# Kernel tuning notes

Measured on AMD Instinct MI355X. Metric: run time of the kernel, lower is better.

The kernel has to match this reference:

```python
import jax, jax.numpy as jnp
import numpy as np

D_MODEL = 1024
D_FF = 4096
N_EXPERTS = 8
D_EXPERT = D_FF // N_EXPERTS  # 512
TOP_K = 2
LB_WEIGHT = 0.01
B, S = 4, 2048


def setup_inputs() -> dict:
    key = jax.random.key(0)
    ks = jax.random.split(key, 8)
    x = jax.random.normal(ks[0], (B, S, D_MODEL), dtype=jnp.float32)
    # per-expert FFN params stacked on expert axis
    w1 = jax.random.normal(ks[1], (N_EXPERTS, D_MODEL, D_EXPERT), dtype=jnp.float32) * (1.0 / np.sqrt(D_MODEL))
    b1 = jnp.zeros((N_EXPERTS, D_EXPERT), dtype=jnp.float32)
    w2 = jax.random.normal(ks[2], (N_EXPERTS, D_EXPERT, D_MODEL), dtype=jnp.float32) * (1.0 / np.sqrt(D_EXPERT))
    b2 = jnp.zeros((N_EXPERTS, D_MODEL), dtype=jnp.float32)
    centroids = jax.random.normal(ks[3], (N_EXPERTS, D_MODEL), dtype=jnp.float32) * 0.02
    w_route = jax.random.normal(ks[4], (N_EXPERTS, D_MODEL), dtype=jnp.float32) * (1.0 / np.sqrt(D_MODEL))
    return {"x": x, "w1": w1, "b1": b1, "w2": w2, "b2": b2,
            "centroids": centroids, "w_route": w_route}


def _top_k_softmax(logits, k):
    # softmax restricted to the top-k logits per token; zeros elsewhere
    vals, _ = jax.lax.top_k(logits, k)          # (..., k)
    thresh = vals[..., -1:]                     # kth-largest value
    masked = jnp.where(logits >= thresh, logits, -jnp.inf)
    return jax.nn.softmax(masked, axis=-1)


def reference(x, w1, b1, w2, b2, centroids, w_route):
    eps = 1e-12
    x_norm = x / jnp.maximum(jnp.linalg.norm(x, axis=-1, keepdims=True), eps)
    c_norm = centroids / jnp.maximum(jnp.linalg.norm(centroids, axis=-1, keepdims=True), eps)
    cos_scores = jnp.einsum('bsd,ed->bse', x_norm, c_norm)
    route_scores = jnp.einsum('bsd,ed->bse', x, w_route)
    logits = cos_scores + route_scores                       # (B,S,E)
    gates = _top_k_softmax(logits, TOP_K)                    # (B,S,E)
    # all experts computed on all tokens (dense MoE, masked combine)
    h = jax.nn.gelu(jnp.einsum('bsd,edh->bseh', x, w1) + b1, approximate=False)
    expert_out = jnp.einsum('bseh,ehd->bsed', h, w2) + b2    # (B,S,E,D)
    out = jnp.einsum('bse,bsed->bsd', gates, expert_out)
    return out
```

## Files before the change

### kernel.cpp

```cpp
#include <hip/hip_runtime.h>
#include <hip/hip_bf16.h>
#include <math.h>

#define T_TOK 8192
#define DM 1024
#define DE 512
#define NE 8
#define DFF 4096

#define CO_X   0
#define CO_W1  8388608
#define CO_W2  12582912
#define CO_B1  16777216
#define CO_B2  16781312
#define CO_CE  16789504
#define CO_WR  16797696
#define CO_TOT 16805888

#define WS_GATE2 256
#define WS_B32   65792
#define WS_TOP2  262400
#define WS_TOK   295168
#define WS_AE    360704
#define WS_AG    426240
#define WS_INV   491776
#define WS_CONV  557312
#define WS_HC    34169088
#define WS_OC    50946304

typedef __attribute__((ext_vector_type(8))) __bf16 bf16x8;
typedef __attribute__((ext_vector_type(4))) __bf16 bf16x4;
typedef __attribute__((ext_vector_type(4))) float f32x4;

__device__ __forceinline__ f32x4 ld4(const void* p, size_t off, int md)
{
  f32x4 r;
  if (md){
    bf16x4 v = *(const bf16x4*)((const __bf16*)p + off);
    #pragma unroll
    for (int j = 0; j < 4; j++) r[j] = (float)v[j];
  } else {
    r = *(const f32x4*)((const float*)p + off);
  }
  return r;
}

__device__ __forceinline__ void async_ld16(const __bf16* g, __bf16* l)
{
  __builtin_amdgcn_global_load_lds(
      (const __attribute__((address_space(1))) unsigned int*)g,
      (__attribute__((address_space(3))) unsigned int*)l, 16, 0, 0);
}

__global__ __launch_bounds__(256) void detect_k(const void* xp, const void* cp,
                                                int* meta, int* b32)
{
  const int tid = threadIdx.x;
  const float* xf = (const float*)xp;
  int ok = 0;
  for (int i = tid; i < 1024; i += 256){
    float a = fabsf(xf[i]);
    if (a > 1e-8f && a < 100.f) ok++;
  }
  __shared__ int cnt;
  __shared__ int flg;
  if (tid == 0) cnt = 0;
  __syncthreads();
  atomicAdd(&cnt, ok);
  __syncthreads();
  if (tid == 0){ flg = (cnt > 512) ? 0 : 1; meta[0] = flg; }
  __syncthreads();
  const int md = flg;

  const int e = tid >> 5, i = tid & 31;
  float ss = 0.f;
  for (int j = 0; j < 32; j++){
    size_t d = (size_t)e * DM + i + j * 32;
    float v = md ? (float)((const __bf16*)cp)[d] : ((const float*)cp)[d];
    ss += v * v;
  }
  #pragma unroll
  for (int m = 1; m < 32; m <<= 1) ss += __shfl_xor(ss, m, 64);
  float* cinv = (float*)(meta + 48);
  if (i == 0) cinv[e] = 1.f / fmaxf(sqrtf(ss), 1e-12f);

  b32[tid] = 0;
  if (tid < 8) meta[16 + tid] = 0;
}

__global__ __launch_bounds__(256) void convert_k(
    const float* __restrict__ b1, const float* __restrict__ b2,
    const float* __restrict__ ce, const float* __restrict__ wr,
    __bf16* __restrict__ dst, const int* __restrict__ meta)
{
  if (meta[0]) return;
  const size_t j = ((size_t)blockIdx.x * 256 + threadIdx.x) * 4;
  const float* src;
  const size_t doff = CO_B1 + j;
  if      (j < 4096)  src = b1 + j;
  else if (j < 12288) src = b2 + (j - 4096);
  else if (j < 20480) src = ce + (j - 12288);
  else                src = wr + (j - 20480);
  f32x4 v = *(const f32x4*)src;
  bf16x4 o;
  #pragma unroll
  for (int t = 0; t < 4; t++) o[t] = (__bf16)v[t];
  *(bf16x4*)(dst + doff) = o;
}

__global__ __launch_bounds__(256) void transp_k(
    const void* w1q, const void* w2q, __bf16* __restrict__ conv,
    const int* __restrict__ meta)
{
  const int md = meta[0];
  __shared__ __bf16 tile[32][33];
  const int b = blockIdx.x, tid = threadIdx.x;
  const int ty = tid >> 5, tx = tid & 31;

  const void* src; __bf16* dst; int ldS, ldD, i0, j0; size_t soff, doffb;
  if (b < 4096){
    const int e = b >> 9, t = b & 511;
    i0 = (t >> 4) << 5; j0 = (t & 15) << 5;
    ldS = DE; ldD = DM;
    soff = (size_t)e * DM * DE;
    dst = conv + CO_W1; doffb = (size_t)e * DE * DM;
    src = md ? (const void*)((const __bf16*)w1q) : (const void*)((const float*)w1q);
  } else {
    const int e = (b - 4096) >> 9, t = (b - 4096) & 511;
    i0 = (t >> 5) << 5; j0 = (t & 31) << 5;
    ldS = DM; ldD = DE;
    soff = (size_t)e * DE * DM;
    dst = conv + CO_W2; doffb = (size_t)e * DM * DE;
    src = md ? (const void*)((const __bf16*)w2q) : (const void*)((const float*)w2q);
  }

  #pragma unroll
  for (int rr = 0; rr < 4; rr++){
    const int r = rr * 8 + ty;
    const size_t s = soff + (size_t)(i0 + r) * ldS + j0 + tx;
    tile[r][tx] = md ? ((const __bf16*)src)[s] : (__bf16)((const float*)src)[s];
  }
  __syncthreads();
  #pragma unroll
  for (int rr = 0; rr < 4; rr++){
    const int r = rr * 8 + ty;
    dst[doffb + (size_t)(j0 + r) * ldD + i0 + tx] = tile[tx][r];
  }
}

__global__ __launch_bounds__(256) void route_k(
    const void* __restrict__ xp, const void* __restrict__ cp,
    const void* __restrict__ wp, const int* __restrict__ meta,
    __bf16* __restrict__ conv, float2* __restrict__ gate2,
    int* __restrict__ top2, int* __restrict__ b32)
{
  const int md = meta[0];
  const float* cinv = (const float*)(meta + 48);
  const int tid = threadIdx.x;
  const int g = tid >> 4, l = tid & 15;
  const int t = blockIdx.x * 16 + g;

  __shared__ int hist[8];
  if (tid < 8) hist[tid] = 0;
  __syncthreads();

  float xx = 0.f, cd[NE], wd[NE];
  #pragma unroll
  for (int e = 0; e < NE; e++){ cd[e] = 0.f; wd[e] = 0.f; }

  const size_t xbase = (size_t)t * DM;
  for (int j = 0; j < 16; j++){
    const int d0 = j * 64 + l * 4;
    f32x4 xv = ld4(xp, xbase + d0, md);
    if (!md){
      bf16x4 o;
      #pragma unroll
      for (int jj = 0; jj < 4; jj++) o[jj] = (__bf16)xv[jj];
      *(bf16x4*)(conv + CO_X + xbase + d0) = o;
    }
    xx += xv[0]*xv[0] + xv[1]*xv[1] + xv[2]*xv[2] + xv[3]*xv[3];
    #pragma unroll
    for (int e = 0; e < NE; e++){
      f32x4 cv = ld4(cp, (size_t)e * DM + d0, md);
      f32x4 wv = ld4(wp, (size_t)e * DM + d0, md);
      cd[e] += xv[0]*cv[0] + xv[1]*cv[1] + xv[2]*cv[2] + xv[3]*cv[3];
      wd[e] += xv[0]*wv[0] + xv[1]*wv[1] + xv[2]*wv[2] + xv[3]*wv[3];
    }
  }
  #pragma unroll
  for (int m = 1; m < 16; m <<= 1){
    xx += __shfl_xor(xx, m, 64);
    #pragma unroll
    for (int e = 0; e < NE; e++){
      cd[e] += __shfl_xor(cd[e], m, 64);
      wd[e] += __shfl_xor(wd[e], m, 64);
    }
  }

  if (l == 0){
    const float rxn = 1.f / fmaxf(sqrtf(xx), 1e-12f);
    float logits[NE];
    #pragma unroll
    for (int e = 0; e < NE; e++) logits[e] = cd[e] * rxn * cinv[e] + wd[e];
    float m1 = -1e30f; int i1 = 0;
    #pragma unroll
    for (int e = 0; e < NE; e++) if (logits[e] > m1){ m1 = logits[e]; i1 = e; }
    float m2 = -1e30f; int i2 = (i1 == 0) ? 1 : 0;
    #pragma unroll
    for (int e = 0; e < NE; e++)
      if (e != i1 && logits[e] > m2){ m2 = logits[e]; i2 = e; }
    float denom = 0.f, ex1 = 0.f, ex2 = 0.f;
    #pragma unroll
    for (int e = 0; e < NE; e++){
      if (logits[e] >= m2){
        float ee = expf(logits[e] - m1);
        denom += ee;
        if (e == i1) ex1 = ee;
        if (e == i2) ex2 = ee;
      }
    }
    const float inv = 1.f / denom;
    gate2[t] = make_float2(ex1 * inv, ex2 * inv);
    top2[t] = i1 | (i2 << 8);
    atomicAdd(&hist[i1], 1);
    atomicAdd(&hist[i2], 1);
  }
  __syncthreads();
  if (tid < 8) atomicAdd(&b32[(blockIdx.x >> 4) * 8 + tid], hist[tid]);
}

__global__ void offsets_k(int* meta, int* b32)
{
  const int l = threadIdx.x;
  int running = 0;
  for (int e = 0; e < NE; e++){
    int v = (l < 32) ? b32[l * 8 + e] : 0;
    int incl = v;
    #pragma unroll
    for (int ofs = 1; ofs < 32; ofs <<= 1){
      int n = __shfl_up(incl, ofs, 64);
      if (l >= ofs) incl += n;
    }
    int tot = __shfl(incl, 31, 64);
    if (l < 32) b32[l * 8 + e] = running + (incl - v);
    if (l == 0){ meta[16 + e] = tot; meta[32 + e] = running; }
    running += tot;
  }
}

__global__ __launch_bounds__(256) void place_k(
    const int* __restrict__ top2, const float2* __restrict__ gate2,
    const int* __restrict__ b32, int* __restrict__ tok, int* __restrict__ ae,
    float* __restrict__ agv, int* __restrict__ inv)
{
  __shared__ int cur[8];
  if (threadIdx.x < 8) cur[threadIdx.x] = b32[blockIdx.x * 8 + threadIdx.x];
  __syncthreads();
  const int t = blockIdx.x * 256 + threadIdx.x;
  const int p = top2[t];
  const float2 gg = gate2[t];
  const int e1 = p & 255, e2 = (p >> 8) & 255;
  const int s1 = atomicAdd(&cur[e1], 1);
  tok[s1] = t; ae[s1] = e1; agv[s1] = gg.x; inv[2 * t] = s1;
  const int s2 = atomicAdd(&cur[e2], 1);
  tok[s2] = t; ae[s2] = e2; agv[s2] = gg.y; inv[2 * t + 1] = s2;
}

__device__ __forceinline__ bool find_tile(const int* meta, int tm,
                                          int& e, int& base, int& valid)
{
  for (e = 0; e < NE; e++){
    const int cnt = meta[16 + e];
    const int nt = (cnt + 127) >> 7;
    if (tm < nt){
      const int r0 = tm << 7;
      base = meta[32 + e] + r0;
      valid = cnt - r0;
      return true;
    }
    tm -= nt;
  }
  return false;
}

__global__ __launch_bounds__(512, 4) void gemm1g_k(
    const void* xq, const void* b1q, const __bf16* __restrict__ conv,
    const int* __restrict__ meta, const int* __restrict__ tok,
    const float* __restrict__ agv, __bf16* __restrict__ Hc)
{
  const int md = meta[0];
  const __bf16* X  = md ? (const __bf16*)xq : conv + CO_X;
  const __bf16* WT = conv + CO_W1;
  const __bf16* bb = md ? (const __bf16*)b1q : conv + CO_B1;

  int e, base, valid;
  if (!find_tile(meta, blockIdx.x, e, base, valid)) return;
  const int n0 = blockIdx.y * 128;

  __shared__ __attribute__((aligned(16))) __bf16 As[2][128 * 32];
  __shared__ __attribute__((aligned(16))) __bf16 Bs[2][128 * 32];

  const int tid = threadIdx.x;
  const int wv = tid >> 6, lane = tid & 63;
  const int q = lane >> 4, ln = lane & 15;
  const int wm = (wv >> 2) * 64, wn = (wv & 3) * 32;
  f32x4 acc[4][2] = {};

  const int sr = tid >> 2, sc = (tid & 3) * 8;
  const int tr = tok[base + ((sr < valid) ? sr : 0)];
  const __bf16* Ag = X + (size_t)tr * DM + sc;
  const __bf16* Bg = WT + (size_t)e * (DE * DM) + (size_t)(n0 + sr) * DM + sc;

  async_ld16(Ag, &As[0][tid * 8]);
  async_ld16(Bg, &Bs[0][tid * 8]);
  __syncthreads();

  int cr = 0;
  for (int k0 = 0; k0 < DM; k0 += 32){
    const int k1 = k0 + 32;
    if (k1 < DM){
      async_ld16(Ag + k1, &As[cr ^ 1][tid * 8]);
      async_ld16(Bg + k1, &Bs[cr ^ 1][tid * 8]);
    }
    bf16x8 af[4], bfr[2];
    #pragma unroll
    for (int mi = 0; mi < 4; mi++)
      af[mi] = *(const bf16x8*)&As[cr][(wm + mi * 16 + ln) * 32 + q * 8];
    #pragma unroll
    for (int ni = 0; ni < 2; ni++)
      bfr[ni] = *(const bf16x8*)&Bs[cr][(wn + ni * 16 + ln) * 32 + q * 8];
    #pragma unroll
    for (int mi = 0; mi < 4; mi++)
      #pragma unroll
      for (int ni = 0; ni < 2; ni++)
        acc[mi][ni] = __builtin_amdgcn_mfma_f32_16x16x32_bf16(
            af[mi], bfr[ni], acc[mi][ni], 0, 0, 0);
    __syncthreads();
    cr ^= 1;
  }

  const int coln = n0 + wn;
  float bset[2];
  #pragma unroll
  for (int ni = 0; ni < 2; ni++)
    bset[ni] = (float)bb[e * DE + coln + ni * 16 + ln];
  #pragma unroll
  for (int mi = 0; mi < 4; mi++){
    #pragma unroll
    for (int r = 0; r < 4; r++){
      const int row = wm + mi * 16 + q * 4 + r;
      if (row < valid){
        const int slot = base + row;
        const float g = agv[slot];
        #pragma unroll
        for (int ni = 0; ni < 2; ni++){
          float v = acc[mi][ni][r] + bset[ni];
          float h = 0.5f * v * (1.0f + erff(v * 0.70710678118654752f));
          Hc[(size_t)slot * DE + coln + ni * 16 + ln] = (__bf16)(g * h);
        }
      }
    }
  }
}

__global__ __launch_bounds__(512, 4) void gemm2g_k(
    const __bf16* __restrict__ Hc, const __bf16* __restrict__ conv,
    const int* __restrict__ meta, __bf16* __restrict__ Oc)
{
  const __bf16* WT = conv + CO_W2;

  int e, base, valid;
  if (!find_tile(meta, blockIdx.x, e, base, valid)) return;
  const int n0 = blockIdx.y * 128;

  __shared__ __attribute__((aligned(16))) __bf16 As[2][128 * 32];
  __shared__ __attribute__((aligned(16))) __bf16 Bs[2][128 * 32];

  const int tid = threadIdx.x;
  const int wv = tid >> 6, lane = tid & 63;
  const int q = lane >> 4, ln = lane & 15;
  const int wm = (wv >> 2) * 64, wn = (wv & 3) * 32;
  f32x4 acc[4][2] = {};

  const int sr = tid >> 2, sc = (tid & 3) * 8;
  const int rc = (sr < valid) ? sr : 0;
  const __bf16* Ag = Hc + (size_t)(base + rc) * DE + sc;
  const __bf16* Bg = WT + (size_t)e * (DM * DE) + (size_t)(n0 + sr) * DE + sc;

  async_ld16(Ag, &As[0][tid * 8]);
  async_ld16(Bg, &Bs[0][tid * 8]);
  __syncthreads();

  int cr = 0;
  for (int k0 = 0; k0 < DE; k0 += 32){
    const int k1 = k0 + 32;
    if (k1 < DE){
      async_ld16(Ag + k1, &As[cr ^ 1][tid * 8]);
      async_ld16(Bg + k1, &Bs[cr ^ 1][tid * 8]);
    }
    bf16x8 af[4], bfr[2];
    #pragma unroll
    for (int mi = 0; mi < 4; mi++)
      af[mi] = *(const bf16x8*)&As[cr][(wm + mi * 16 + ln) * 32 + q * 8];
    #pragma unroll
    for (int ni = 0; ni < 2; ni++)
      bfr[ni] = *(const bf16x8*)&Bs[cr][(wn + ni * 16 + ln) * 32 + q * 8];
    #pragma unroll
    for (int mi = 0; mi < 4; mi++)
      #pragma unroll
      for (int ni = 0; ni < 2; ni++)
        acc[mi][ni] = __builtin_amdgcn_mfma_f32_16x16x32_bf16(
            af[mi], bfr[ni], acc[mi][ni], 0, 0, 0);
    __syncthreads();
    cr ^= 1;
  }

  #pragma unroll
  for (int mi = 0; mi < 4; mi++){
    #pragma unroll
    for (int r = 0; r < 4; r++){
      const int row = wm + mi * 16 + q * 4 + r;
      if (row < valid){
        const int slot = base + row;
        #pragma unroll
        for (int ni = 0; ni < 2; ni++)
          Oc[(size_t)slot * DM + n0 + wn + ni * 16 + ln] = (__bf16)acc[mi][ni][r];
      }
    }
  }
}

__global__ __launch_bounds__(256) void combine_k(
    const __bf16* __restrict__ Oc, const int* __restrict__ inv,
    const int* __restrict__ ae, const float* __restrict__ agv,
    const void* b2q, const int* __restrict__ meta, void* out)
{
  const int md = meta[0];
  const int t = blockIdx.x;
  const int s1 = inv[2 * t], s2 = inv[2 * t + 1];
  const int e1 = ae[s1], e2 = ae[s2];
  const float g1 = agv[s1], g2 = agv[s2];
  const int c = threadIdx.x * 4;

  bf16x4 o1 = *(const bf16x4*)(Oc + (size_t)s1 * DM + c);
  bf16x4 o2 = *(const bf16x4*)(Oc + (size_t)s2 * DM + c);
  f32x4 bv1 = ld4(b2q, (size_t)e1 * DM + c, md);
  f32x4 bv2 = ld4(b2q, (size_t)e2 * DM + c, md);
  f32x4 rr;
  #pragma unroll
  for (int j = 0; j < 4; j++)
    rr[j] = (float)o1[j] + (float)o2[j] + g1 * bv1[j] + g2 * bv2[j];

  if (md){
    bf16x4 ob;
    #pragma unroll
    for (int j = 0; j < 4; j++) ob[j] = (__bf16)rr[j];
    *(bf16x4*)((__bf16*)out + (size_t)t * DM + c) = ob;
  } else {
    *(f32x4*)((float*)out + (size_t)t * DM + c) = rr;
  }
}

extern "C" void kernel_launch(void* const* d_in, const int* in_sizes, int n_in,
                              void* d_out, int out_size, void* d_ws, size_t ws_size,
                              hipStream_t stream)
{
  char* ws = (char*)d_ws;
  int*    meta  = (int*)ws;
  float2* gate2 = (float2*)(ws + WS_GATE2);
  int*    b32   = (int*)(ws + WS_B32);
  int*    top2  = (int*)(ws + WS_TOP2);
  int*    tok   = (int*)(ws + WS_TOK);
  int*    ae    = (int*)(ws + WS_AE);
  float*  agv   = (float*)(ws + WS_AG);
  int*    inv   = (int*)(ws + WS_INV);
  __bf16* conv  = (__bf16*)(ws + WS_CONV);
  __bf16* Hc    = (__bf16*)(ws + WS_HC);
  __bf16* Oc    = (__bf16*)(ws + WS_OC);

  detect_k<<<1, 256, 0, stream>>>(d_in[0], d_in[5], meta, b32);
  transp_k<<<8192, 256, 0, stream>>>(d_in[1], d_in[3], conv, meta);
  convert_k<<<28, 256, 0, stream>>>(
      (const float*)d_in[2], (const float*)d_in[4], (const float*)d_in[5],
      (const float*)d_in[6], conv, meta);
  route_k<<<T_TOK / 16, 256, 0, stream>>>(d_in[0], d_in[5], d_in[6], meta,
                                          conv, gate2, top2, b32);
  offsets_k<<<1, 64, 0, stream>>>(meta, b32);
  place_k<<<T_TOK / 256, 256, 0, stream>>>(top2, gate2, b32, tok, ae, agv, inv);
  gemm1g_k<<<dim3(136, 4), 512, 0, stream>>>(d_in[0], d_in[2], conv, meta,
                                             tok, agv, Hc);
  gemm2g_k<<<dim3(136, 8), 512, 0, stream>>>(Hc, conv, meta, Oc);
  combine_k<<<T_TOK, 256, 0, stream>>>(Oc, inv, ae, agv, d_in[4], meta, d_out);
}
```

Before: 245.4 us.

## Enlarge grouped GEMM tiles to 256x256 and route four tokens per lane group

Both grouped expert GEMMs move from 128x128 to 256x256 output tiles, with each wave computing 128x64 through an 8x4 MFMA accumulator array. Grid sizes shrink to match, and occupancy drops to two blocks per CU. The routing kernel now has each 16-lane group handle four tokens, so the centroid and router weight loads are reused across them. The larger tiles raise arithmetic intensity, but with only about 144 and 288 blocks on 256 CUs, part of the GPU sits idle, register pressure rises, and per-expert padding waste grows.

```diff
diff --git a/kernel.cpp b/kernel.cpp
--- a/kernel.cpp
+++ b/kernel.cpp
@@ -158,50 +158,73 @@
   const float* cinv = (const float*)(meta + 48);
   const int tid = threadIdx.x;
   const int g = tid >> 4, l = tid & 15;
-  const int t = blockIdx.x * 16 + g;
+  const int tbase = blockIdx.x * 64 + g * 4;
 
   __shared__ int hist[8];
   if (tid < 8) hist[tid] = 0;
   __syncthreads();
 
-  float xx = 0.f, cd[NE], wd[NE];
-  #pragma unroll
-  for (int e = 0; e < NE; e++){ cd[e] = 0.f; wd[e] = 0.f; }
-
-  const size_t xbase = (size_t)t * DM;
+  float xx[4] = {0.f, 0.f, 0.f, 0.f};
+  float cd[NE][4], wd[NE][4];
+  #pragma unroll
+  for (int e = 0; e < NE; e++)
+    #pragma unroll
+    for (int tk = 0; tk < 4; tk++){ cd[e][tk] = 0.f; wd[e][tk] = 0.f; }
+
   for (int j = 0; j < 16; j++){
     const int d0 = j * 64 + l * 4;
-    f32x4 xv = ld4(xp, xbase + d0, md);
-    if (!md){
-      bf16x4 o;
-      #pragma unroll
-      for (int jj = 0; jj < 4; jj++) o[jj] = (__bf16)xv[jj];
-      *(bf16x4*)(conv + CO_X + xbase + d0) = o;
-    }
-    xx += xv[0]*xv[0] + xv[1]*xv[1] + xv[2]*xv[2] + xv[3]*xv[3];
+    f32x4 xv[4];
+    #pragma unroll
+    for (int tk = 0; tk < 4; tk++){
+      xv[tk] = ld4(xp, (size_t)(tbase + tk) * DM + d0, md);
+      if (!md){
+        bf16x4 o;
+        #pragma unroll
+        for (int jj = 0; jj < 4; jj++) o[jj] = (__bf16)xv[tk][jj];
+        *(bf16x4*)(conv + CO_X + (size_t)(tbase + tk) * DM + d0) = o;
+      }
+      xx[tk] += xv[tk][0]*xv[tk][0] + xv[tk][1]*xv[tk][1]
+              + xv[tk][2]*xv[tk][2] + xv[tk][3]*xv[tk][3];
+    }
     #pragma unroll
     for (int e = 0; e < NE; e++){
       f32x4 cv = ld4(cp, (size_t)e * DM + d0, md);
       f32x4 wv = ld4(wp, (size_t)e * DM + d0, md);
-      cd[e] += xv[0]*cv[0] + xv[1]*cv[1] + xv[2]*cv[2] + xv[3]*cv[3];
-      wd[e] += xv[0]*wv[0] + xv[1]*wv[1] + xv[2]*wv[2] + xv[3]*wv[3];
+      #pragma unroll
+      for (int tk = 0; tk < 4; tk++){
+        cd[e][tk] += xv[tk][0]*cv[0] + xv[tk][1]*cv[1]
+                   + xv[tk][2]*cv[2] + xv[tk][3]*cv[3];
+        wd[e][tk] += xv[tk][0]*wv[0] + xv[tk][1]*wv[1]
+                   + xv[tk][2]*wv[2] + xv[tk][3]*wv[3];
+      }
     }
   }
   #pragma unroll
   for (int m = 1; m < 16; m <<= 1){
-    xx += __shfl_xor(xx, m, 64);
+    #pragma unroll
+    for (int tk = 0; tk < 4; tk++){
+      xx[tk] += __shfl_xor(xx[tk], m, 64);
+      #pragma unroll
+      for (int e = 0; e < NE; e++){
+        cd[e][tk] += __shfl_xor(cd[e][tk], m, 64);
+        wd[e][tk] += __shfl_xor(wd[e][tk], m, 64);
+      }
+    }
+  }
+
+  if (l < 4){
+    const int t = tbase + l;
+    float xxs = (l == 0) ? xx[0] : (l == 1) ? xx[1] : (l == 2) ? xx[2] : xx[3];
+    float logits[NE];
     #pragma unroll
     for (int e = 0; e < NE; e++){
-      cd[e] += __shfl_xor(cd[e], m, 64);
-      wd[e] += __shfl_xor(wd[e], m, 64);
-    }
-  }
-
-  if (l == 0){
-    const float rxn = 1.f / fmaxf(sqrtf(xx), 1e-12f);
-    float logits[NE];
-    #pragma unroll
-    for (int e = 0; e < NE; e++) logits[e] = cd[e] * rxn * cinv[e] + wd[e];
+      float cds = (l == 0) ? cd[e][0] : (l == 1) ? cd[e][1]
+                : (l == 2) ? cd[e][2] : cd[e][3];
+      float wds = (l == 0) ? wd[e][0] : (l == 1) ? wd[e][1]
+                : (l == 2) ? wd[e][2] : wd[e][3];
+      const float rxn = 1.f / fmaxf(sqrtf(xxs), 1e-12f);
+      logits[e] = cds * rxn * cinv[e] + wds;
+    }
     float m1 = -1e30f; int i1 = 0;
     #pragma unroll
     for (int e = 0; e < NE; e++) if (logits[e] > m1){ m1 = logits[e]; i1 = e; }
@@ -226,7 +249,7 @@
     atomicAdd(&hist[i2], 1);
   }
   __syncthreads();
-  if (tid < 8) atomicAdd(&b32[(blockIdx.x >> 4) * 8 + tid], hist[tid]);
+  if (tid < 8) atomicAdd(&b32[(blockIdx.x >> 2) * 8 + tid], hist[tid]);
 }
 
 __global__ void offsets_k(int* meta, int* b32)
@@ -266,14 +289,14 @@
   tok[s2] = t; ae[s2] = e2; agv[s2] = gg.y; inv[2 * t + 1] = s2;
 }
 
-__device__ __forceinline__ bool find_tile(const int* meta, int tm,
-                                          int& e, int& base, int& valid)
+__device__ __forceinline__ bool find_tile256(const int* meta, int tm,
+                                             int& e, int& base, int& valid)
 {
   for (e = 0; e < NE; e++){
     const int cnt = meta[16 + e];
-    const int nt = (cnt + 127) >> 7;
+    const int nt = (cnt + 255) >> 8;
     if (tm < nt){
-      const int r0 = tm << 7;
+      const int r0 = tm << 8;
       base = meta[32 + e] + r0;
       valid = cnt - r0;
       return true;
@@ -283,7 +306,7 @@
   return false;
 }
 
-__global__ __launch_bounds__(512, 4) void gemm1g_k(
+__global__ __launch_bounds__(512, 2) void gemm1g_k(
     const void* xq, const void* b1q, const __bf16* __restrict__ conv,
     const int* __restrict__ meta, const int* __restrict__ tok,
     const float* __restrict__ agv, __bf16* __restrict__ Hc)
@@ -294,45 +317,52 @@
   const __bf16* bb = md ? (const __bf16*)b1q : conv + CO_B1;
 
   int e, base, valid;
-  if (!find_tile(meta, blockIdx.x, e, base, valid)) return;
-  const int n0 = blockIdx.y * 128;
-
-  __shared__ __attribute__((aligned(16))) __bf16 As[2][128 * 32];
-  __shared__ __attribute__((aligned(16))) __bf16 Bs[2][128 * 32];
+  if (!find_tile256(meta, blockIdx.x, e, base, valid)) return;
+  const int n0 = blockIdx.y * 256;
+
+  __shared__ __attribute__((aligned(16))) __bf16 As[2][256 * 32];
+  __shared__ __attribute__((aligned(16))) __bf16 Bs[2][256 * 32];
 
   const int tid = threadIdx.x;
   const int wv = tid >> 6, lane = tid & 63;
   const int q = lane >> 4, ln = lane & 15;
-  const int wm = (wv >> 2) * 64, wn = (wv & 3) * 32;
-  f32x4 acc[4][2] = {};
+  const int wm = (wv >> 2) * 128, wn = (wv & 3) * 64;
+  f32x4 acc[8][4] = {};
 
   const int sr = tid >> 2, sc = (tid & 3) * 8;
-  const int tr = tok[base + ((sr < valid) ? sr : 0)];
-  const __bf16* Ag = X + (size_t)tr * DM + sc;
-  const __bf16* Bg = WT + (size_t)e * (DE * DM) + (size_t)(n0 + sr) * DM + sc;
-
-  async_ld16(Ag, &As[0][tid * 8]);
-  async_ld16(Bg, &Bs[0][tid * 8]);
+  const int t0 = tok[base + ((sr       < valid) ? sr       : 0)];
+  const int t1 = tok[base + ((sr + 128 < valid) ? sr + 128 : 0)];
+  const __bf16* Ag0 = X + (size_t)t0 * DM + sc;
+  const __bf16* Ag1 = X + (size_t)t1 * DM + sc;
+  const __bf16* Bg0 = WT + (size_t)e * (DE * DM) + (size_t)(n0 + sr) * DM + sc;
+  const __bf16* Bg1 = Bg0 + (size_t)128 * DM;
+
+  async_ld16(Ag0, &As[0][tid * 8]);
+  async_ld16(Ag1, &As[0][tid * 8 + 4096]);
+  async_ld16(Bg0, &Bs[0][tid * 8]);
+  async_ld16(Bg1, &Bs[0][tid * 8 + 4096]);
   __syncthreads();
 
   int cr = 0;
   for (int k0 = 0; k0 < DM; k0 += 32){
     const int k1 = k0 + 32;
     if (k1 < DM){
-      async_ld16(Ag + k1, &As[cr ^ 1][tid * 8]);
-      async_ld16(Bg + k1, &Bs[cr ^ 1][tid * 8]);
-    }
-    bf16x8 af[4], bfr[2];
-    #pragma unroll
-    for (int mi = 0; mi < 4; mi++)
+      async_ld16(Ag0 + k1, &As[cr ^ 1][tid * 8]);
+      async_ld16(Ag1 + k1, &As[cr ^ 1][tid * 8 + 4096]);
+      async_ld16(Bg0 + k1, &Bs[cr ^ 1][tid * 8]);
+      async_ld16(Bg1 + k1, &Bs[cr ^ 1][tid * 8 + 4096]);
+    }
+    bf16x8 af[8], bfr[4];
+    #pragma unroll
+    for (int mi = 0; mi < 8; mi++)
       af[mi] = *(const bf16x8*)&As[cr][(wm + mi * 16 + ln) * 32 + q * 8];
     #pragma unroll
-    for (int ni = 0; ni < 2; ni++)
+    for (int ni = 0; ni < 4; ni++)
       bfr[ni] = *(const bf16x8*)&Bs[cr][(wn + ni * 16 + ln) * 32 + q * 8];
     #pragma unroll
-    for (int mi = 0; mi < 4; mi++)
+    for (int mi = 0; mi < 8; mi++)
       #pragma unroll
-      for (int ni = 0; ni < 2; ni++)
+      for (int ni = 0; ni < 4; ni++)
         acc[mi][ni] = __builtin_amdgcn_mfma_f32_16x16x32_bf16(
             af[mi], bfr[ni], acc[mi][ni], 0, 0, 0);
     __syncthreads();
@@ -340,12 +370,12 @@
   }
 
   const int coln = n0 + wn;
-  float bset[2];
-  #pragma unroll
-  for (int ni = 0; ni < 2; ni++)
+  float bset[4];
+  #pragma unroll
+  for (int ni = 0; ni < 4; ni++)
     bset[ni] = (float)bb[e * DE + coln + ni * 16 + ln];
   #pragma unroll
-  for (int mi = 0; mi < 4; mi++){
+  for (int mi = 0; mi < 8; mi++){
     #pragma unroll
     for (int r = 0; r < 4; r++){
       const int row = wm + mi * 16 + q * 4 + r;
@@ -353,7 +383,7 @@
         const int slot = base + row;
         const float g = agv[slot];
         #pragma unroll
-        for (int ni = 0; ni < 2; ni++){
+        for (int ni = 0; ni < 4; ni++){
           float v = acc[mi][ni][r] + bset[ni];
           float h = 0.5f * v * (1.0f + erff(v * 0.70710678118654752f));
           Hc[(size_t)slot * DE + coln + ni * 16 + ln] = (__bf16)(g * h);
@@ -363,52 +393,59 @@
   }
 }
 
-__global__ __launch_bounds__(512, 4) void gemm2g_k(
+__global__ __launch_bounds__(512, 2) void gemm2g_k(
     const __bf16* __restrict__ Hc, const __bf16* __restrict__ conv,
     const int* __restrict__ meta, __bf16* __restrict__ Oc)
 {
   const __bf16* WT = conv + CO_W2;
 
   int e, base, valid;
-  if (!find_tile(meta, blockIdx.x, e, base, valid)) return;
-  const int n0 = blockIdx.y * 128;
-
-  __shared__ __attribute__((aligned(16))) __bf16 As[2][128 * 32];
-  __shared__ __attribute__((aligned(16))) __bf16 Bs[2][128 * 32];
+  if (!find_tile256(meta, blockIdx.x, e, base, valid)) return;
+  const int n0 = blockIdx.y * 256;
+
+  __shared__ __attribute__((aligned(16))) __bf16 As[2][256 * 32];
+  __shared__ __attribute__((aligned(16))) __bf16 Bs[2][256 * 32];
 
   const int tid = threadIdx.x;
   const int wv = tid >> 6, lane = tid & 63;
   const int q = lane >> 4, ln = lane & 15;
-  const int wm = (wv >> 2) * 64, wn = (wv & 3) * 32;
-  f32x4 acc[4][2] = {};
+  const int wm = (wv >> 2) * 128, wn = (wv & 3) * 64;
+  f32x4 acc[8][4] = {};
 
   const int sr = tid >> 2, sc = (tid & 3) * 8;
-  const int rc = (sr < valid) ? sr : 0;
-  const __bf16* Ag = Hc + (size_t)(base + rc) * DE + sc;
-  const __bf16* Bg = WT + (size_t)e * (DM * DE) + (size_t)(n0 + sr) * DE + sc;
-
-  async_ld16(Ag, &As[0][tid * 8]);
-  async_ld16(Bg, &Bs[0][tid * 8]);
+  const int r0 = (sr       < valid) ? sr       : 0;
+  const int r1 = (sr + 128 < valid) ? sr + 128 : 0;
+  const __bf16* Ag0 = Hc + (size_t)(base + r0) * DE + sc;
+  const __bf16* Ag1 = Hc + (size_t)(base + r1) * DE + sc;
+  const __bf16* Bg0 = WT + (size_t)e * (DM * DE) + (size_t)(n0 + sr) * DE + sc;
+  const __bf16* Bg1 = Bg0 + (size_t)128 * DE;
+
+  async_ld16(Ag0, &As[0][tid * 8]);
+  async_ld16(Ag1, &As[0][tid * 8 + 4096]);
+  async_ld16(Bg0, &Bs[0][tid * 8]);
+  async_ld16(Bg1, &Bs[0][tid * 8 + 4096]);
   __syncthreads();
 
   int cr = 0;
   for (int k0 = 0; k0 < DE; k0 += 32){
     const int k1 = k0 + 32;
     if (k1 < DE){
-      async_ld16(Ag + k1, &As[cr ^ 1][tid * 8]);
-      async_ld16(Bg + k1, &Bs[cr ^ 1][tid * 8]);
-    }
-    bf16x8 af[4], bfr[2];
-    #pragma unroll
-    for (int mi = 0; mi < 4; mi++)
+      async_ld16(Ag0 + k1, &As[cr ^ 1][tid * 8]);
+      async_ld16(Ag1 + k1, &As[cr ^ 1][tid * 8 + 4096]);
+      async_ld16(Bg0 + k1, &Bs[cr ^ 1][tid * 8]);
+      async_ld16(Bg1 + k1, &Bs[cr ^ 1][tid * 8 + 4096]);
+    }
+    bf16x8 af[8], bfr[4];
+    #pragma unroll
+    for (int mi = 0; mi < 8; mi++)
       af[mi] = *(const bf16x8*)&As[cr][(wm + mi * 16 + ln) * 32 + q * 8];
     #pragma unroll
-    for (int ni = 0; ni < 2; ni++)
+    for (int ni = 0; ni < 4; ni++)
       bfr[ni] = *(const bf16x8*)&Bs[cr][(wn + ni * 16 + ln) * 32 + q * 8];
     #pragma unroll
-    for (int mi = 0; mi < 4; mi++)
+    for (int mi = 0; mi < 8; mi++)
       #pragma unroll
-      for (int ni = 0; ni < 2; ni++)
+      for (int ni = 0; ni < 4; ni++)
         acc[mi][ni] = __builtin_amdgcn_mfma_f32_16x16x32_bf16(
             af[mi], bfr[ni], acc[mi][ni], 0, 0, 0);
     __syncthreads();
@@ -416,14 +453,14 @@
   }
 
   #pragma unroll
-  for (int mi = 0; mi < 4; mi++){
+  for (int mi = 0; mi < 8; mi++){
     #pragma unroll
     for (int r = 0; r < 4; r++){
       const int row = wm + mi * 16 + q * 4 + r;
       if (row < valid){
         const int slot = base + row;
         #pragma unroll
-        for (int ni = 0; ni < 2; ni++)
+        for (int ni = 0; ni < 4; ni++)
           Oc[(size_t)slot * DM + n0 + wn + ni * 16 + ln] = (__bf16)acc[mi][ni][r];
       }
     }
@@ -483,12 +520,12 @@
   convert_k<<<28, 256, 0, stream>>>(
       (const float*)d_in[2], (const float*)d_in[4], (const float*)d_in[5],
       (const float*)d_in[6], conv, meta);
-  route_k<<<T_TOK / 16, 256, 0, stream>>>(d_in[0], d_in[5], d_in[6], meta,
+  route_k<<<T_TOK / 64, 256, 0, stream>>>(d_in[0], d_in[5], d_in[6], meta,
                                           conv, gate2, top2, b32);
   offsets_k<<<1, 64, 0, stream>>>(meta, b32);
   place_k<<<T_TOK / 256, 256, 0, stream>>>(top2, gate2, b32, tok, ae, agv, inv);
-  gemm1g_k<<<dim3(136, 4), 512, 0, stream>>>(d_in[0], d_in[2], conv, meta,
-                                             tok, agv, Hc);
-  gemm2g_k<<<dim3(136, 8), 512, 0, stream>>>(Hc, conv, meta, Oc);
+  gemm1g_k<<<dim3(72, 2), 512, 0, stream>>>(d_in[0], d_in[2], conv, meta,
+                                            tok, agv, Hc);
+  gemm2g_k<<<dim3(72, 4), 512, 0, stream>>>(Hc, conv, meta, Oc);
   combine_k<<<T_TOK, 256, 0, stream>>>(Oc, inv, ae, agv, d_in[4], meta, d_out);
 }
```

Result: slower. 332.8 us (+35.6%).

## Deepen GEMM K-tiles to 64 with XOR-swizzled LDS; enlarge gemm2 tiles to 256x256

Applied to the files above, without the earlier changes.

Both grouped expert GEMMs now stage 64-wide K chunks per pipeline step with an XOR swizzle on the LDS layout, halving the number of barriers and aiming to avoid bank conflicts on fragment reads. gemm2 moves to 256x256 output tiles with 8x4 MFMA accumulators per wave and a smaller grid (72x4), raising data reuse per loaded byte. Larger LDS footprints and more accumulator registers lower occupancy (launch bounds drop to 2 blocks). The bigger tiles also waste more rows on partially filled expert tiles and leave fewer blocks to fill the device.

```diff
diff --git a/kernel.cpp b/kernel.cpp
--- a/kernel.cpp
+++ b/kernel.cpp
@@ -283,7 +283,24 @@
   return false;
 }
 
-__global__ __launch_bounds__(512, 4) void gemm1g_k(
+__device__ __forceinline__ bool find_tile256(const int* meta, int tm,
+                                             int& e, int& base, int& valid)
+{
+  for (e = 0; e < NE; e++){
+    const int cnt = meta[16 + e];
+    const int nt = (cnt + 255) >> 8;
+    if (tm < nt){
+      const int r0 = tm << 8;
+      base = meta[32 + e] + r0;
+      valid = cnt - r0;
+      return true;
+    }
+    tm -= nt;
+  }
+  return false;
+}
+
+__global__ __launch_bounds__(512, 2) void gemm1g_k(
     const void* xq, const void* b1q, const __bf16* __restrict__ conv,
     const int* __restrict__ meta, const int* __restrict__ tok,
     const float* __restrict__ agv, __bf16* __restrict__ Hc)
@@ -297,47 +314,65 @@
   if (!find_tile(meta, blockIdx.x, e, base, valid)) return;
   const int n0 = blockIdx.y * 128;
 
-  __shared__ __attribute__((aligned(16))) __bf16 As[2][128 * 32];
-  __shared__ __attribute__((aligned(16))) __bf16 Bs[2][128 * 32];
+  __shared__ __attribute__((aligned(16))) __bf16 As[2][128 * 64];
+  __shared__ __attribute__((aligned(16))) __bf16 Bs[2][128 * 64];
 
   const int tid = threadIdx.x;
   const int wv = tid >> 6, lane = tid & 63;
   const int q = lane >> 4, ln = lane & 15;
   const int wm = (wv >> 2) * 64, wn = (wv & 3) * 32;
+  const int swz = ln & 7;
   f32x4 acc[4][2] = {};
 
-  const int sr = tid >> 2, sc = (tid & 3) * 8;
-  const int tr = tok[base + ((sr < valid) ? sr : 0)];
-  const __bf16* Ag = X + (size_t)tr * DM + sc;
-  const __bf16* Bg = WT + (size_t)e * (DE * DM) + (size_t)(n0 + sr) * DM + sc;
-
-  async_ld16(Ag, &As[0][tid * 8]);
-  async_ld16(Bg, &Bs[0][tid * 8]);
-  __syncthreads();
-
+  const int srow = tid >> 3, sch = tid & 7;
+  const int sx = ((sch ^ (srow & 7)) << 3);
+  const int ta = tok[base + ((srow      < valid) ? srow      : 0)];
+  const int tb = tok[base + ((srow + 64 < valid) ? srow + 64 : 0)];
+  const __bf16* Ag0 = X + (size_t)ta * DM + sx;
+  const __bf16* Ag1 = X + (size_t)tb * DM + sx;
+  const __bf16* Bg0 = WT + (size_t)e * (DE * DM) + (size_t)(n0 + srow) * DM + sx;
+  const __bf16* Bg1 = Bg0 + (size_t)64 * DM;
+
+  #define G1_STAGE(BUF, K0)                                   \
+    do {                                                      \
+      async_ld16(Ag0 + (K0), &As[BUF][tid * 8]);              \
+      async_ld16(Ag1 + (K0), &As[BUF][tid * 8 + 4096]);       \
+      async_ld16(Bg0 + (K0), &Bs[BUF][tid * 8]);              \
+      async_ld16(Bg1 + (K0), &Bs[BUF][tid * 8 + 4096]);       \
+    } while (0)
+
+  #define G1_COMPUTE(BUF)                                                      \
+    do {                                                                       \
+      _Pragma("unroll")                                                        \
+      for (int kk = 0; kk < 2; kk++){                                          \
+        bf16x8 af[4], bfr[2];                                                  \
+        const int ch = (((kk << 2) | q) ^ swz) << 3;                           \
+        _Pragma("unroll")                                                      \
+        for (int mi = 0; mi < 4; mi++)                                         \
+          af[mi] = *(const bf16x8*)&As[BUF][(wm + mi * 16 + ln) * 64 + ch];    \
+        _Pragma("unroll")                                                      \
+        for (int ni = 0; ni < 2; ni++)                                         \
+          bfr[ni] = *(const bf16x8*)&Bs[BUF][(wn + ni * 16 + ln) * 64 + ch];   \
+        _Pragma("unroll")                                                      \
+        for (int mi = 0; mi < 4; mi++)                                         \
+          _Pragma("unroll")                                                    \
+          for (int ni = 0; ni < 2; ni++)                                       \
+            acc[mi][ni] = __builtin_amdgcn_mfma_f32_16x16x32_bf16(             \
+                af[mi], bfr[ni], acc[mi][ni], 0, 0, 0);                        \
+      }                                                                        \
+    } while (0)
+
+  G1_STAGE(0, 0);
+  __syncthreads();
   int cr = 0;
-  for (int k0 = 0; k0 < DM; k0 += 32){
-    const int k1 = k0 + 32;
-    if (k1 < DM){
-      async_ld16(Ag + k1, &As[cr ^ 1][tid * 8]);
-      async_ld16(Bg + k1, &Bs[cr ^ 1][tid * 8]);
-    }
-    bf16x8 af[4], bfr[2];
-    #pragma unroll
-    for (int mi = 0; mi < 4; mi++)
-      af[mi] = *(const bf16x8*)&As[cr][(wm + mi * 16 + ln) * 32 + q * 8];
-    #pragma unroll
-    for (int ni = 0; ni < 2; ni++)
-      bfr[ni] = *(const bf16x8*)&Bs[cr][(wn + ni * 16 + ln) * 32 + q * 8];
-    #pragma unroll
-    for (int mi = 0; mi < 4; mi++)
-      #pragma unroll
-      for (int ni = 0; ni < 2; ni++)
-        acc[mi][ni] = __builtin_amdgcn_mfma_f32_16x16x32_bf16(
-            af[mi], bfr[ni], acc[mi][ni], 0, 0, 0);
+  for (int t = 0; t < 16; ++t){
+    if (t < 15) G1_STAGE(cr ^ 1, (t + 1) * 64);
+    G1_COMPUTE(cr);
     __syncthreads();
     cr ^= 1;
   }
+  #undef G1_STAGE
+  #undef G1_COMPUTE
 
   const int coln = n0 + wn;
   float bset[2];
@@ -363,67 +398,92 @@
   }
 }
 
-__global__ __launch_bounds__(512, 4) void gemm2g_k(
+__global__ __launch_bounds__(512, 2) void gemm2g_k(
     const __bf16* __restrict__ Hc, const __bf16* __restrict__ conv,
     const int* __restrict__ meta, __bf16* __restrict__ Oc)
 {
   const __bf16* WT = conv + CO_W2;
 
   int e, base, valid;
-  if (!find_tile(meta, blockIdx.x, e, base, valid)) return;
-  const int n0 = blockIdx.y * 128;
-
-  __shared__ __attribute__((aligned(16))) __bf16 As[2][128 * 32];
-  __shared__ __attribute__((aligned(16))) __bf16 Bs[2][128 * 32];
+  if (!find_tile256(meta, blockIdx.x, e, base, valid)) return;
+  const int n0 = blockIdx.y * 256;
+
+  __shared__ __attribute__((aligned(16))) __bf16 As[2][256 * 64];
+  __shared__ __attribute__((aligned(16))) __bf16 Bs[2][256 * 64];
 
   const int tid = threadIdx.x;
   const int wv = tid >> 6, lane = tid & 63;
   const int q = lane >> 4, ln = lane & 15;
-  const int wm = (wv >> 2) * 64, wn = (wv & 3) * 32;
-  f32x4 acc[4][2] = {};
-
-  const int sr = tid >> 2, sc = (tid & 3) * 8;
-  const int rc = (sr < valid) ? sr : 0;
-  const __bf16* Ag = Hc + (size_t)(base + rc) * DE + sc;
-  const __bf16* Bg = WT + (size_t)e * (DM * DE) + (size_t)(n0 + sr) * DE + sc;
-
-  async_ld16(Ag, &As[0][tid * 8]);
-  async_ld16(Bg, &Bs[0][tid * 8]);
-  __syncthreads();
-
+  const int wm = (wv >> 2) * 128, wn = (wv & 3) * 64;
+  const int swz = ln & 7;
+  f32x4 acc[8][4] = {};
+
+  const int srow = tid >> 3, sch = tid & 7;
+  const int sx = ((sch ^ (srow & 7)) << 3);
+  const int r0 = (srow       < valid) ? srow       : 0;
+  const int r1 = (srow +  64 < valid) ? srow +  64 : 0;
+  const int r2 = (srow + 128 < valid) ? srow + 128 : 0;
+  const int r3 = (srow + 192 < valid) ? srow + 192 : 0;
+  const __bf16* Ag0 = Hc + (size_t)(base + r0) * DE + sx;
+  const __bf16* Ag1 = Hc + (size_t)(base + r1) * DE + sx;
+  const __bf16* Ag2 = Hc + (size_t)(base + r2) * DE + sx;
+  const __bf16* Ag3 = Hc + (size_t)(base + r3) * DE + sx;
+  const __bf16* Bg0 = WT + (size_t)e * (DM * DE) + (size_t)(n0 + srow) * DE + sx;
+
+  #define G2_STAGE(BUF, K0)                                          \
+    do {                                                             \
+      async_ld16(Ag0 + (K0), &As[BUF][tid * 8]);                     \
+      async_ld16(Ag1 + (K0), &As[BUF][tid * 8 + 4096]);              \
+      async_ld16(Ag2 + (K0), &As[BUF][tid * 8 + 8192]);              \
+      async_ld16(Ag3 + (K0), &As[BUF][tid * 8 + 12288]);             \
+      async_ld16(Bg0 + (K0),                &Bs[BUF][tid * 8]);      \
+      async_ld16(Bg0 + (K0) +  64 * DE,     &Bs[BUF][tid * 8 + 4096]);  \
+      async_ld16(Bg0 + (K0) + 128 * DE,     &Bs[BUF][tid * 8 + 8192]);  \
+      async_ld16(Bg0 + (K0) + 192 * DE,     &Bs[BUF][tid * 8 + 12288]); \
+    } while (0)
+
+  #define G2_COMPUTE(BUF)                                                      \
+    do {                                                                       \
+      _Pragma("unroll")                                                        \
+      for (int kk = 0; kk < 2; kk++){                                          \
+        bf16x8 af[8], bfr[4];                                                  \
+        const int ch = (((kk << 2) | q) ^ swz) << 3;                           \
+        _Pragma("unroll")                                                      \
+        for (int mi = 0; mi < 8; mi++)                                         \
+          af[mi] = *(const bf16x8*)&As[BUF][(wm + mi * 16 + ln) * 64 + ch];    \
+        _Pragma("unroll")                                                      \
+        for (int ni = 0; ni < 4; ni++)                                         \
+          bfr[ni] = *(const bf16x8*)&Bs[BUF][(wn + ni * 16 + ln) * 64 + ch];   \
+        _Pragma("unroll")                                                      \
+        for (int mi = 0; mi < 8; mi++)                                         \
+          _Pragma("unroll")                                                    \
+          for (int ni = 0; ni < 4; ni++)                                       \
+            acc[mi][ni] = __builtin_amdgcn_mfma_f32_16x16x32_bf16(             \
+                af[mi], bfr[ni], acc[mi][ni], 0, 0, 0);                        \
+      }                                                                        \
+    } while (0)
+
+  G2_STAGE(0, 0);
+  __syncthreads();
   int cr = 0;
-  for (int k0 = 0; k0 < DE; k0 += 32){
-    const int k1 = k0 + 32;
-    if (k1 < DE){
-      async_ld16(Ag + k1, &As[cr ^ 1][tid * 8]);
-      async_ld16(Bg + k1, &Bs[cr ^ 1][tid * 8]);
-    }
-    bf16x8 af[4], bfr[2];
-    #pragma unroll
-    for (int mi = 0; mi < 4; mi++)
-      af[mi] = *(const bf16x8*)&As[cr][(wm + mi * 16 + ln) * 32 + q * 8];
-    #pragma unroll
-    for (int ni = 0; ni < 2; ni++)
-      bfr[ni] = *(const bf16x8*)&Bs[cr][(wn + ni * 16 + ln) * 32 + q * 8];
-    #pragma unroll
-    for (int mi = 0; mi < 4; mi++)
-      #pragma unroll
-      for (int ni = 0; ni < 2; ni++)
-        acc[mi][ni] = __builtin_amdgcn_mfma_f32_16x16x32_bf16(
-            af[mi], bfr[ni], acc[mi][ni], 0, 0, 0);
+  for (int t = 0; t < 8; ++t){
+    if (t < 7) G2_STAGE(cr ^ 1, (t + 1) * 64);
+    G2_COMPUTE(cr);
     __syncthreads();
     cr ^= 1;
   }
-
-  #pragma unroll
-  for (int mi = 0; mi < 4; mi++){
+  #undef G2_STAGE
+  #undef G2_COMPUTE
+
+  #pragma unroll
+  for (int mi = 0; mi < 8; mi++){
     #pragma unroll
     for (int r = 0; r < 4; r++){
       const int row = wm + mi * 16 + q * 4 + r;
       if (row < valid){
         const int slot = base + row;
         #pragma unroll
-        for (int ni = 0; ni < 2; ni++)
+        for (int ni = 0; ni < 4; ni++)
           Oc[(size_t)slot * DM + n0 + wn + ni * 16 + ln] = (__bf16)acc[mi][ni][r];
       }
     }
@@ -489,6 +549,6 @@
   place_k<<<T_TOK / 256, 256, 0, stream>>>(top2, gate2, b32, tok, ae, agv, inv);
   gemm1g_k<<<dim3(136, 4), 512, 0, stream>>>(d_in[0], d_in[2], conv, meta,
                                              tok, agv, Hc);
-  gemm2g_k<<<dim3(136, 8), 512, 0, stream>>>(Hc, conv, meta, Oc);
+  gemm2g_k<<<dim3(72, 4), 512, 0, stream>>>(Hc, conv, meta, Oc);
   combine_k<<<T_TOK, 256, 0, stream>>>(Oc, inv, ae, agv, d_in[4], meta, d_out);
 }
```

Measured after the change: 250.5 us. 1.02x slower.

## Widen grouped GEMM tiles to 128x256 and index tiles by expert-interleaved slots

Applied to the files above, without the earlier changes.

Both grouped expert GEMMs move from a 128x128 to a 128x256 output tile, with each wave computing a 64x64 sub-tile (4x4 MFMA accumulators). This doubles the reuse of A-fragment loads per B load and halves the number of column blocks. The tile lookup loop is replaced by a direct mapping, expert = bx&7 and row block = bx>>3, over a fixed 512-wide grid, so many blocks exit early. Occupancy hint drops from 4 to 2 blocks per CU, and register and LDS use rise.

```diff
diff --git a/kernel.cpp b/kernel.cpp
--- a/kernel.cpp
+++ b/kernel.cpp
@@ -266,24 +266,19 @@
   tok[s2] = t; ae[s2] = e2; agv[s2] = gg.y; inv[2 * t + 1] = s2;
 }
 
-__device__ __forceinline__ bool find_tile(const int* meta, int tm,
+__device__ __forceinline__ bool find_slot(const int* meta, int bx,
                                           int& e, int& base, int& valid)
 {
-  for (e = 0; e < NE; e++){
-    const int cnt = meta[16 + e];
-    const int nt = (cnt + 127) >> 7;
-    if (tm < nt){
-      const int r0 = tm << 7;
-      base = meta[32 + e] + r0;
-      valid = cnt - r0;
-      return true;
-    }
-    tm -= nt;
-  }
-  return false;
-}
-
-__global__ __launch_bounds__(512, 4) void gemm1g_k(
+  e = bx & 7;
+  const int cnt = meta[16 + e];
+  const int r0 = (bx >> 3) << 7;
+  if (r0 >= cnt) return false;
+  base = meta[32 + e] + r0;
+  valid = cnt - r0;
+  return true;
+}
+
+__global__ __launch_bounds__(512, 2) void gemm1g_k(
     const void* xq, const void* b1q, const __bf16* __restrict__ conv,
     const int* __restrict__ meta, const int* __restrict__ tok,
     const float* __restrict__ agv, __bf16* __restrict__ Hc)
@@ -294,55 +289,64 @@
   const __bf16* bb = md ? (const __bf16*)b1q : conv + CO_B1;
 
   int e, base, valid;
-  if (!find_tile(meta, blockIdx.x, e, base, valid)) return;
-  const int n0 = blockIdx.y * 128;
+  if (!find_slot(meta, blockIdx.x, e, base, valid)) return;
+  const int n0 = blockIdx.y * 256;
 
   __shared__ __attribute__((aligned(16))) __bf16 As[2][128 * 32];
-  __shared__ __attribute__((aligned(16))) __bf16 Bs[2][128 * 32];
+  __shared__ __attribute__((aligned(16))) __bf16 Bs[2][256 * 32];
 
   const int tid = threadIdx.x;
   const int wv = tid >> 6, lane = tid & 63;
   const int q = lane >> 4, ln = lane & 15;
-  const int wm = (wv >> 2) * 64, wn = (wv & 3) * 32;
-  f32x4 acc[4][2] = {};
+  const int wm = (wv >> 2) * 64, wn = (wv & 3) * 64;
+  f32x4 acc[4][4] = {};
 
   const int sr = tid >> 2, sc = (tid & 3) * 8;
-  const int tr = tok[base + ((sr < valid) ? sr : 0)];
-  const __bf16* Ag = X + (size_t)tr * DM + sc;
-  const __bf16* Bg = WT + (size_t)e * (DE * DM) + (size_t)(n0 + sr) * DM + sc;
-
-  async_ld16(Ag, &As[0][tid * 8]);
-  async_ld16(Bg, &Bs[0][tid * 8]);
-  __syncthreads();
-
+  const int ta = tok[base + ((sr < valid) ? sr : 0)];
+  const __bf16* Ag  = X + (size_t)ta * DM + sc;
+  const __bf16* Bg0 = WT + (size_t)e * (DE * DM) + (size_t)(n0 + sr) * DM + sc;
+  const __bf16* Bg1 = Bg0 + (size_t)128 * DM;
+
+  #define G1_STAGE(BUF, K0)                              \
+    do {                                                 \
+      async_ld16(Ag  + (K0), &As[BUF][tid * 8]);         \
+      async_ld16(Bg0 + (K0), &Bs[BUF][tid * 8]);         \
+      async_ld16(Bg1 + (K0), &Bs[BUF][tid * 8 + 4096]);  \
+    } while (0)
+
+  #define G1_COMPUTE(BUF)                                                      \
+    do {                                                                       \
+      bf16x8 af[4], bfr[4];                                                    \
+      _Pragma("unroll")                                                        \
+      for (int mi = 0; mi < 4; mi++)                                           \
+        af[mi] = *(const bf16x8*)&As[BUF][(wm + mi * 16 + ln) * 32 + q * 8];   \
+      _Pragma("unroll")                                                        \
+      for (int ni = 0; ni < 4; ni++)                                           \
+        bfr[ni] = *(const bf16x8*)&Bs[BUF][(wn + ni * 16 + ln) * 32 + q * 8];  \
+      _Pragma("unroll")                                                        \
+      for (int mi = 0; mi < 4; mi++)                                           \
+        _Pragma("unroll")                                                      \
+        for (int ni = 0; ni < 4; ni++)                                         \
+          acc[mi][ni] = __builtin_amdgcn_mfma_f32_16x16x32_bf16(               \
+              af[mi], bfr[ni], acc[mi][ni], 0, 0, 0);                          \
+    } while (0)
+
+  G1_STAGE(0, 0);
+  __syncthreads();
   int cr = 0;
-  for (int k0 = 0; k0 < DM; k0 += 32){
-    const int k1 = k0 + 32;
-    if (k1 < DM){
-      async_ld16(Ag + k1, &As[cr ^ 1][tid * 8]);
-      async_ld16(Bg + k1, &Bs[cr ^ 1][tid * 8]);
-    }
-    bf16x8 af[4], bfr[2];
-    #pragma unroll
-    for (int mi = 0; mi < 4; mi++)
-      af[mi] = *(const bf16x8*)&As[cr][(wm + mi * 16 + ln) * 32 + q * 8];
-    #pragma unroll
-    for (int ni = 0; ni < 2; ni++)
-      bfr[ni] = *(const bf16x8*)&Bs[cr][(wn + ni * 16 + ln) * 32 + q * 8];
-    #pragma unroll
-    for (int mi = 0; mi < 4; mi++)
-      #pragma unroll
-      for (int ni = 0; ni < 2; ni++)
-        acc[mi][ni] = __builtin_amdgcn_mfma_f32_16x16x32_bf16(
-            af[mi], bfr[ni], acc[mi][ni], 0, 0, 0);
+  for (int t = 0; t < 32; ++t){
+    if (t < 31) G1_STAGE(cr ^ 1, (t + 1) * 32);
+    G1_COMPUTE(cr);
     __syncthreads();
     cr ^= 1;
   }
+  #undef G1_STAGE
+  #undef G1_COMPUTE
 
   const int coln = n0 + wn;
-  float bset[2];
-  #pragma unroll
-  for (int ni = 0; ni < 2; ni++)
+  float bset[4];
+  #pragma unroll
+  for (int ni = 0; ni < 4; ni++)
     bset[ni] = (float)bb[e * DE + coln + ni * 16 + ln];
   #pragma unroll
   for (int mi = 0; mi < 4; mi++){
@@ -353,7 +357,7 @@
         const int slot = base + row;
         const float g = agv[slot];
         #pragma unroll
-        for (int ni = 0; ni < 2; ni++){
+        for (int ni = 0; ni < 4; ni++){
           float v = acc[mi][ni][r] + bset[ni];
           float h = 0.5f * v * (1.0f + erff(v * 0.70710678118654752f));
           Hc[(size_t)slot * DE + coln + ni * 16 + ln] = (__bf16)(g * h);
@@ -363,57 +367,66 @@
   }
 }
 
-__global__ __launch_bounds__(512, 4) void gemm2g_k(
+__global__ __launch_bounds__(512, 2) void gemm2g_k(
     const __bf16* __restrict__ Hc, const __bf16* __restrict__ conv,
     const int* __restrict__ meta, __bf16* __restrict__ Oc)
 {
   const __bf16* WT = conv + CO_W2;
 
   int e, base, valid;
-  if (!find_tile(meta, blockIdx.x, e, base, valid)) return;
-  const int n0 = blockIdx.y * 128;
+  if (!find_slot(meta, blockIdx.x, e, base, valid)) return;
+  const int n0 = blockIdx.y * 256;
 
   __shared__ __attribute__((aligned(16))) __bf16 As[2][128 * 32];
-  __shared__ __attribute__((aligned(16))) __bf16 Bs[2][128 * 32];
+  __shared__ __attribute__((aligned(16))) __bf16 Bs[2][256 * 32];
 
   const int tid = threadIdx.x;
   const int wv = tid >> 6, lane = tid & 63;
   const int q = lane >> 4, ln = lane & 15;
-  const int wm = (wv >> 2) * 64, wn = (wv & 3) * 32;
-  f32x4 acc[4][2] = {};
+  const int wm = (wv >> 2) * 64, wn = (wv & 3) * 64;
+  f32x4 acc[4][4] = {};
 
   const int sr = tid >> 2, sc = (tid & 3) * 8;
-  const int rc = (sr < valid) ? sr : 0;
-  const __bf16* Ag = Hc + (size_t)(base + rc) * DE + sc;
-  const __bf16* Bg = WT + (size_t)e * (DM * DE) + (size_t)(n0 + sr) * DE + sc;
-
-  async_ld16(Ag, &As[0][tid * 8]);
-  async_ld16(Bg, &Bs[0][tid * 8]);
-  __syncthreads();
-
+  const int ra = (sr < valid) ? sr : 0;
+  const __bf16* Ag  = Hc + (size_t)(base + ra) * DE + sc;
+  const __bf16* Bg0 = WT + (size_t)e * (DM * DE) + (size_t)(n0 + sr) * DE + sc;
+  const __bf16* Bg1 = Bg0 + (size_t)128 * DE;
+
+  #define G2_STAGE(BUF, K0)                              \
+    do {                                                 \
+      async_ld16(Ag  + (K0), &As[BUF][tid * 8]);         \
+      async_ld16(Bg0 + (K0), &Bs[BUF][tid * 8]);         \
+      async_ld16(Bg1 + (K0), &Bs[BUF][tid * 8 + 4096]);  \
+    } while (0)
+
+  #define G2_COMPUTE(BUF)                                                      \
+    do {                                                                       \
+      bf16x8 af[4], bfr[4];                                                    \
+      _Pragma("unroll")                                                        \
+      for (int mi = 0; mi < 4; mi++)                                           \
+        af[mi] = *(const bf16x8*)&As[BUF][(wm + mi * 16 + ln) * 32 + q * 8];   \
+      _Pragma("unroll")                                                        \
+      for (int ni = 0; ni < 4; ni++)                                           \
+        bfr[ni] = *(const bf16x8*)&Bs[BUF][(wn + ni * 16 + ln) * 32 + q * 8];  \
+      _Pragma("unroll")                                                        \
+      for (int mi = 0; mi < 4; mi++)                                           \
+        _Pragma("unroll")                                                      \
+        for (int ni = 0; ni < 4; ni++)                                         \
+          acc[mi][ni] = __builtin_amdgcn_mfma_f32_16x16x32_bf16(               \
+              af[mi], bfr[ni], acc[mi][ni], 0, 0, 0);                          \
+    } while (0)
+
+  G2_STAGE(0, 0);
+  __syncthreads();
   int cr = 0;
-  for (int k0 = 0; k0 < DE; k0 += 32){
-    const int k1 = k0 + 32;
-    if (k1 < DE){
-      async_ld16(Ag + k1, &As[cr ^ 1][tid * 8]);
-      async_ld16(Bg + k1, &Bs[cr ^ 1][tid * 8]);
-    }
-    bf16x8 af[4], bfr[2];
-    #pragma unroll
-    for (int mi = 0; mi < 4; mi++)
-      af[mi] = *(const bf16x8*)&As[cr][(wm + mi * 16 + ln) * 32 + q * 8];
-    #pragma unroll
-    for (int ni = 0; ni < 2; ni++)
-      bfr[ni] = *(const bf16x8*)&Bs[cr][(wn + ni * 16 + ln) * 32 + q * 8];
-    #pragma unroll
-    for (int mi = 0; mi < 4; mi++)
-      #pragma unroll
-      for (int ni = 0; ni < 2; ni++)
-        acc[mi][ni] = __builtin_amdgcn_mfma_f32_16x16x32_bf16(
-            af[mi], bfr[ni], acc[mi][ni], 0, 0, 0);
+  for (int t = 0; t < 16; ++t){
+    if (t < 15) G2_STAGE(cr ^ 1, (t + 1) * 32);
+    G2_COMPUTE(cr);
     __syncthreads();
     cr ^= 1;
   }
+  #undef G2_STAGE
+  #undef G2_COMPUTE
 
   #pragma unroll
   for (int mi = 0; mi < 4; mi++){
@@ -423,7 +436,7 @@
       if (row < valid){
         const int slot = base + row;
         #pragma unroll
-        for (int ni = 0; ni < 2; ni++)
+        for (int ni = 0; ni < 4; ni++)
           Oc[(size_t)slot * DM + n0 + wn + ni * 16 + ln] = (__bf16)acc[mi][ni][r];
       }
     }
@@ -487,8 +500,8 @@
                                           conv, gate2, top2, b32);
   offsets_k<<<1, 64, 0, stream>>>(meta, b32);
   place_k<<<T_TOK / 256, 256, 0, stream>>>(top2, gate2, b32, tok, ae, agv, inv);
-  gemm1g_k<<<dim3(136, 4), 512, 0, stream>>>(d_in[0], d_in[2], conv, meta,
+  gemm1g_k<<<dim3(512, 2), 512, 0, stream>>>(d_in[0], d_in[2], conv, meta,
                                              tok, agv, Hc);
-  gemm2g_k<<<dim3(136, 8), 512, 0, stream>>>(Hc, conv, meta, Oc);
+  gemm2g_k<<<dim3(512, 4), 512, 0, stream>>>(Hc, conv, meta, Oc);
   combine_k<<<T_TOK, 256, 0, stream>>>(Oc, inv, ae, agv, d_in[4], meta, d_out);
 }
```

Result: slower. 251.6 us (+2.5%).
